# Kernel optimization log

Measured on AMD Instinct MI355X. Metric: run time of the kernel, lower is better.

## Reference

```python
import jax, jax.numpy as jnp
import numpy as np

B, T = 64, 512
IN, OUT, H = 256, 256, 1024


def _lstm_cell(x, h, c, Wih, Whh, bih, bhh):
    # PyTorch LSTMCell: gates = x@Wih^T + bih + h@Whh^T + bhh, order i,f,g,o
    gates = x @ Wih.T + bih + h @ Whh.T + bhh
    i, f, g, o = jnp.split(gates, 4, axis=-1)
    c_new = jax.nn.sigmoid(f) * c + jax.nn.sigmoid(i) * jnp.tanh(g)
    h_new = jax.nn.sigmoid(o) * jnp.tanh(c_new)
    return h_new, c_new


def setup_inputs() -> dict:
    key = jax.random.key(0)
    ks = jax.random.split(key, 12)
    s = 1.0 / np.sqrt(H)  # torch default uniform(-1/sqrt(H), 1/sqrt(H))
    u = lambda k, shp: jax.random.uniform(k, shp, jnp.float32, -s, s)
    return {
        "z": jax.random.normal(ks[0], (B, H), jnp.float32),
        "x": jax.random.normal(ks[1], (B, T, IN), jnp.float32),
        "Wih0": u(ks[2], (4 * H, IN)),
        "Whh0": u(ks[3], (4 * H, H)),
        "bih0": u(ks[4], (4 * H,)),
        "bhh0": u(ks[5], (4 * H,)),
        "Wih1": u(ks[6], (4 * H, H)),
        "Whh1": u(ks[7], (4 * H, H)),
        "bih1": u(ks[8], (4 * H,)),
        "bhh1": u(ks[9], (4 * H,)),
        "Wlin": u(ks[10], (OUT, H)),
        "blin": u(ks[11], (OUT,)),
    }


def reference(z, x, Wih0, Whh0, bih0, bhh0, Wih1, Whh1, bih1, bhh1, Wlin, blin):
    # Teacher-forcing unroll: h_t[l] init to z, c_t[l] init to 0, first input is zeros,
    # then input at step t+1 is x[:, t].
    x_tb = jnp.swapaxes(x, 0, 1)  # [T, B, IN]
    c0_init = jnp.zeros_like(z)

    def step(carry, x_t):
        cur_in, h0, c0, h1, c1 = carry
        h0, c0 = _lstm_cell(cur_in, h0, c0, Wih0, Whh0, bih0, bhh0)
        h1, c1 = _lstm_cell(h0, h1, c1, Wih1, Whh1, bih1, bhh1)
        out_t = h1 @ Wlin.T + blin  # [B, OUT]
        return (x_t, h0, c0, h1, c1), out_t

    init = (jnp.zeros((z.shape[0], Wih0.shape[1]), z.dtype), z, c0_init, z, c0_init)
    _, outs = jax.lax.scan(step, init, x_tb)  # outs: [T, B, OUT]
    return jnp.swapaxes(outs, 0, 1)  # [B, T, OUT]
```

## Files before the change

kernel.cpp:

```cpp
#include <hip/hip_runtime.h>
#include <hip/hip_bf16.h>
#include <math.h>


typedef __attribute__((ext_vector_type(8))) short bf16x8;
typedef __attribute__((ext_vector_type(4))) float f32x4;

__device__ __forceinline__ float sigm(float v) { return 1.f / (1.f + expf(-v)); }

__device__ __forceinline__ void vstore_bf16(__hip_bfloat16* p, float v) {
  __hip_bfloat16 hb = __float2bfloat16(v);
  unsigned short us;
  __builtin_memcpy(&us, &hb, 2);
  *(volatile unsigned short*)p = us;
}


__global__ __launch_bounds__(256) void prep_w0(const float* __restrict__ Wih0,
                                               const float* __restrict__ Whh0,
                                               __hip_bfloat16* __restrict__ W0) {
  const unsigned n = 4096u * 1280u;
  for (unsigned d = blockIdx.x * blockDim.x + threadIdx.x; d < n;
       d += blockDim.x * gridDim.x) {
    unsigned r = d / 1280u;
    unsigned k = d - r * 1280u;
    unsigned u = r >> 2, g = r & 3u;
    unsigned srow = g * 1024u + u;
    float v = (k < 256u) ? Wih0[(size_t)srow * 256u + k]
                         : Whh0[(size_t)srow * 1024u + (k - 256u)];
    W0[d] = __float2bfloat16(v);
  }
}

__global__ __launch_bounds__(256) void prep_w1(const float* __restrict__ Wih1,
                                               const float* __restrict__ Whh1,
                                               const float* __restrict__ Wlin,
                                               __hip_bfloat16* __restrict__ W1) {
  const unsigned n = 4352u * 2048u;
  for (unsigned d = blockIdx.x * blockDim.x + threadIdx.x; d < n;
       d += blockDim.x * gridDim.x) {
    unsigned r = d >> 11;
    unsigned k = d & 2047u;
    float v;
    if (r < 4096u) {
      unsigned u = r >> 2, g = r & 3u;
      unsigned srow = g * 1024u + u;
      v = (k < 1024u) ? Wih1[(size_t)srow * 1024u + k]
                      : Whh1[(size_t)srow * 1024u + (k - 1024u)];
    } else {
      unsigned o = r - 4096u;
      v = (k < 1024u) ? 0.f : Wlin[(size_t)o * 1024u + (k - 1024u)];
    }
    W1[d] = __float2bfloat16(v);
  }
}

__global__ __launch_bounds__(256) void prep_x(const float* __restrict__ x,
                                              __hip_bfloat16* __restrict__ xbf) {
  const unsigned n = 512u * 64u * 256u;
  for (unsigned d = blockIdx.x * blockDim.x + threadIdx.x; d < n;
       d += blockDim.x * gridDim.x) {
    unsigned t = d >> 14;
    unsigned b = (d >> 8) & 63u;
    unsigned k = d & 255u;
    float v = (t == 0u) ? 0.f : x[((size_t)b * 512u + (t - 1u)) * 256u + k];
    xbf[d] = __float2bfloat16(v);
  }
}

__global__ __launch_bounds__(256) void prep_misc(
    const float* __restrict__ bih0, const float* __restrict__ bhh0,
    const float* __restrict__ bih1, const float* __restrict__ bhh1,
    const float* __restrict__ z, float* __restrict__ b0, float* __restrict__ b1,
    __hip_bfloat16* __restrict__ h0buf, __hip_bfloat16* __restrict__ h1buf) {
  for (int i = blockIdx.x * blockDim.x + threadIdx.x; i < 73728;
       i += blockDim.x * gridDim.x) {
    if (i < 4096) {
      int u = i >> 2, g = i & 3;
      b0[i] = bih0[g * 1024 + u] + bhh0[g * 1024 + u];
    } else if (i < 8192) {
      int r = i - 4096;
      int u = r >> 2, g = r & 3;
      b1[r] = bih1[g * 1024 + u] + bhh1[g * 1024 + u];
    } else {
      int j = i - 8192;
      float zv = z[j];
      vstore_bf16(h0buf + j, zv);
      vstore_bf16(h1buf + 2 * 65536 + j, zv);
    }
  }
}


__device__ __forceinline__ void bar_arrive(unsigned* __restrict__ root,
                                           unsigned* __restrict__ lvl,
                                           int phase, int tid) {
  __builtin_amdgcn_s_waitcnt(0);
  __syncthreads();
  if (tid == 0) {
    unsigned old = __hip_atomic_fetch_add(lvl, 1u, __ATOMIC_RELAXED,
                                          __HIP_MEMORY_SCOPE_AGENT);
    if (old == (unsigned)phase * 32u + 31u)
      __hip_atomic_fetch_add(root, 1u, __ATOMIC_RELAXED,
                             __HIP_MEMORY_SCOPE_AGENT);
  }
}

__device__ __forceinline__ void bar_wait(unsigned* __restrict__ root, int phase,
                                         int tid) {
  if (tid == 0) {
    const unsigned tgt = (unsigned)(phase + 1) * 8u;
    while (__hip_atomic_load(root, __ATOMIC_RELAXED,
                             __HIP_MEMORY_SCOPE_AGENT) < tgt)
      __builtin_amdgcn_s_sleep(2);
    __builtin_amdgcn_fence(__ATOMIC_ACQUIRE, "agent");
  }
  __syncthreads();
}


__device__ __forceinline__ void do_proj(const __hip_bfloat16* __restrict__ h1p,
                                        const bf16x8* wp, float (*red)[16][68],
                                        const float* __restrict__ blin,
                                        float* __restrict__ out, int pb,
                                        int t_out, int tid, int w, int col,
                                        int kq) {
  f32x4 a0 = {0.f, 0.f, 0.f, 0.f}, a1 = a0, a2 = a0, a3 = a0;
  const __hip_bfloat16* ab = h1p + (w << 7) + (kq << 3);
#pragma unroll
  for (int c = 0; c < 4; ++c) {
    const __hip_bfloat16* p = ab + (c << 5);
    bf16x8 f0 = *(const bf16x8*)(p + ((size_t)col << 10));
    bf16x8 f1 = *(const bf16x8*)(p + ((size_t)(16 + col) << 10));
    bf16x8 f2 = *(const bf16x8*)(p + ((size_t)(32 + col) << 10));
    bf16x8 f3 = *(const bf16x8*)(p + ((size_t)(48 + col) << 10));
    a0 = __builtin_amdgcn_mfma_f32_16x16x32_bf16(f0, wp[c], a0, 0, 0, 0);
    a1 = __builtin_amdgcn_mfma_f32_16x16x32_bf16(f1, wp[c], a1, 0, 0, 0);
    a2 = __builtin_amdgcn_mfma_f32_16x16x32_bf16(f2, wp[c], a2, 0, 0, 0);
    a3 = __builtin_amdgcn_mfma_f32_16x16x32_bf16(f3, wp[c], a3, 0, 0, 0);
  }
  *(f32x4*)&red[w][col][(kq << 2)] = a0;
  *(f32x4*)&red[w][col][16 + (kq << 2)] = a1;
  *(f32x4*)&red[w][col][32 + (kq << 2)] = a2;
  *(f32x4*)&red[w][col][48 + (kq << 2)] = a3;
  __syncthreads();
#pragma unroll
  for (int i = 0; i < 2; ++i) {
    int idx = tid + (i << 9);
    int o_l = idx & 15, b = idx >> 4;
    float v = blin[(pb << 4) + o_l];
#pragma unroll
    for (int ww = 0; ww < 8; ++ww) v += red[ww][o_l][b];
    out[(((size_t)b << 9) + (size_t)t_out) * 256 + (pb << 4) + o_l] = v;
  }
  __syncthreads();
}


__global__ __launch_bounds__(512) void k_persist(
    const __hip_bfloat16* __restrict__ xbf, const __hip_bfloat16* __restrict__ W0,
    const __hip_bfloat16* __restrict__ W1, const float* __restrict__ b0,
    const float* __restrict__ b1, const float* __restrict__ blin,
    __hip_bfloat16* __restrict__ h0buf, __hip_bfloat16* __restrict__ h1buf,
    float* __restrict__ out, unsigned* __restrict__ bar) {
  const int tid = threadIdx.x;
  const int lane = tid & 63;
  const int w = tid >> 6;
  const int bid = blockIdx.x;
  const int cb = bid << 4;
  const int col = lane & 15;
  const int kq = lane >> 4;
  const int n = cb + col;
  const bool isproj = (bid < 16);

  bf16x8 wa[5], wb[8], wp[4];
  {
    const __hip_bfloat16* p = W0 + (size_t)n * 1280 + w * 160 + (kq << 3);
#pragma unroll
    for (int c = 0; c < 5; ++c) wa[c] = *(const bf16x8*)(p + (c << 5));
  }
  {
    const __hip_bfloat16* p = W1 + ((size_t)n << 11) + (w << 8) + (kq << 3);
#pragma unroll
    for (int c = 0; c < 8; ++c) wb[c] = *(const bf16x8*)(p + (c << 5));
  }
  if (isproj) {
    const __hip_bfloat16* p =
        W1 + ((size_t)(4096 + cb + col) << 11) + 1024 + (w << 7) + (kq << 3);
#pragma unroll
    for (int c = 0; c < 4; ++c) wp[c] = *(const bf16x8*)(p + (c << 5));
  } else {
#pragma unroll
    for (int c = 0; c < 4; ++c) wp[c] = bf16x8{0, 0, 0, 0, 0, 0, 0, 0};
  }

  const int u_l = tid & 3, bq = tid >> 2;
  float bias0[4], bias1[4];
  if (tid < 256) {
#pragma unroll
    for (int g = 0; g < 4; ++g) {
      bias0[g] = b0[cb + (u_l << 2) + g];
      bias1[g] = b1[cb + (u_l << 2) + g];
    }
  }
  float c0v = 0.f, c1v = 0.f;

  __shared__ float red[8][16][68];

  unsigned* lvl = bar + 16 + ((bid & 7) << 6);

  for (int t = 0; t < 512; ++t) {
    const __hip_bfloat16* h0prev = h0buf + ((size_t)(t & 1) << 16);
    const __hip_bfloat16* h0cur = h0buf + ((size_t)((t + 1) & 1) << 16);
    const __hip_bfloat16* h1prev = h1buf + ((size_t)((t + 2) % 3) << 16);
    const __hip_bfloat16* h1proj = h1buf + ((size_t)((t + 1) % 3) << 16);

    {
      f32x4 a0 = {0.f, 0.f, 0.f, 0.f}, a1 = a0, a2 = a0, a3 = a0;
#pragma unroll
      for (int c = 0; c < 5; ++c) {
        const int k0 = w * 160 + (c << 5);
        const __hip_bfloat16* ab;
        size_t rs;
        if (k0 < 256) {
          ab = xbf + ((size_t)t << 14) + k0 + (kq << 3);
          rs = 256;
        } else {
          ab = h0prev + (k0 - 256) + (kq << 3);
          rs = 1024;
        }
        bf16x8 f0 = *(const bf16x8*)(ab + (size_t)col * rs);
        bf16x8 f1 = *(const bf16x8*)(ab + (size_t)(16 + col) * rs);
        bf16x8 f2 = *(const bf16x8*)(ab + (size_t)(32 + col) * rs);
        bf16x8 f3 = *(const bf16x8*)(ab + (size_t)(48 + col) * rs);
        a0 = __builtin_amdgcn_mfma_f32_16x16x32_bf16(f0, wa[c], a0, 0, 0, 0);
        a1 = __builtin_amdgcn_mfma_f32_16x16x32_bf16(f1, wa[c], a1, 0, 0, 0);
        a2 = __builtin_amdgcn_mfma_f32_16x16x32_bf16(f2, wa[c], a2, 0, 0, 0);
        a3 = __builtin_amdgcn_mfma_f32_16x16x32_bf16(f3, wa[c], a3, 0, 0, 0);
      }
      *(f32x4*)&red[w][col][(kq << 2)] = a0;
      *(f32x4*)&red[w][col][16 + (kq << 2)] = a1;
      *(f32x4*)&red[w][col][32 + (kq << 2)] = a2;
      *(f32x4*)&red[w][col][48 + (kq << 2)] = a3;
    }
    __syncthreads();
    if (tid < 256) {
      float gg[4];
#pragma unroll
      for (int g = 0; g < 4; ++g) {
        float v = bias0[g];
#pragma unroll
        for (int ww = 0; ww < 8; ++ww) v += red[ww][(u_l << 2) + g][bq];
        gg[g] = v;
      }
      float cn = sigm(gg[1]) * c0v + sigm(gg[0]) * tanhf(gg[2]);
      c0v = cn;
      float hn = sigm(gg[3]) * tanhf(cn);
      vstore_bf16(h0buf + ((size_t)((t + 1) & 1) << 16) + ((size_t)bq << 10) +
                      (cb >> 2) + u_l,
                  hn);
    }

    bar_arrive(bar, lvl, t, tid);
    if (isproj && t >= 2)
      do_proj(h1proj, wp, red, blin, out, bid, t - 2, tid, w, col, kq);
    bar_wait(bar, t, tid);

    {
      const __hip_bfloat16* ab =
          ((w < 4) ? h0cur : h1prev) + ((w & 3) << 8) + (kq << 3);
      f32x4 a0 = {0.f, 0.f, 0.f, 0.f}, a1 = a0, a2 = a0, a3 = a0;
#pragma unroll
      for (int c = 0; c < 8; ++c) {
        const __hip_bfloat16* p = ab + (c << 5);
        bf16x8 f0 = *(const bf16x8*)(p + ((size_t)col << 10));
        bf16x8 f1 = *(const bf16x8*)(p + ((size_t)(16 + col) << 10));
        bf16x8 f2 = *(const bf16x8*)(p + ((size_t)(32 + col) << 10));
        bf16x8 f3 = *(const bf16x8*)(p + ((size_t)(48 + col) << 10));
        a0 = __builtin_amdgcn_mfma_f32_16x16x32_bf16(f0, wb[c], a0, 0, 0, 0);
        a1 = __builtin_amdgcn_mfma_f32_16x16x32_bf16(f1, wb[c], a1, 0, 0, 0);
        a2 = __builtin_amdgcn_mfma_f32_16x16x32_bf16(f2, wb[c], a2, 0, 0, 0);
        a3 = __builtin_amdgcn_mfma_f32_16x16x32_bf16(f3, wb[c], a3, 0, 0, 0);
      }
      *(f32x4*)&red[w][col][(kq << 2)] = a0;
      *(f32x4*)&red[w][col][16 + (kq << 2)] = a1;
      *(f32x4*)&red[w][col][32 + (kq << 2)] = a2;
      *(f32x4*)&red[w][col][48 + (kq << 2)] = a3;
    }
    __syncthreads();
    if (tid < 256) {
      float gg[4];
#pragma unroll
      for (int g = 0; g < 4; ++g) {
        float v = bias1[g];
#pragma unroll
        for (int ww = 0; ww < 8; ++ww) v += red[ww][(u_l << 2) + g][bq];
        gg[g] = v;
      }
      float cn = sigm(gg[1]) * c1v + sigm(gg[0]) * tanhf(gg[2]);
      c1v = cn;
      float hn = sigm(gg[3]) * tanhf(cn);
      vstore_bf16(h1buf + ((size_t)(t % 3) << 16) + ((size_t)bq << 10) +
                      (cb >> 2) + u_l,
                  hn);
    }
    __syncthreads();
  }

  bar_arrive(bar, lvl, 512, tid);
  bar_wait(bar, 512, tid);
  if (isproj) {
    do_proj(h1buf + ((size_t)(510 % 3) << 16), wp, red, blin, out, bid, 510,
            tid, w, col, kq);
    do_proj(h1buf + ((size_t)(511 % 3) << 16), wp, red, blin, out, bid, 511,
            tid, w, col, kq);
  }
}


extern "C" void kernel_launch(void* const* d_in, const int* in_sizes, int n_in,
                              void* d_out, int out_size, void* d_ws, size_t ws_size,
                              hipStream_t stream) {
  const float* z = (const float*)d_in[0];
  const float* x = (const float*)d_in[1];
  const float* Wih0 = (const float*)d_in[2];
  const float* Whh0 = (const float*)d_in[3];
  const float* bih0 = (const float*)d_in[4];
  const float* bhh0 = (const float*)d_in[5];
  const float* Wih1 = (const float*)d_in[6];
  const float* Whh1 = (const float*)d_in[7];
  const float* bih1 = (const float*)d_in[8];
  const float* bhh1 = (const float*)d_in[9];
  const float* Wlin = (const float*)d_in[10];
  const float* blin = (const float*)d_in[11];
  float* out = (float*)d_out;

  char* ws = (char*)d_ws;
  __hip_bfloat16* W0 = (__hip_bfloat16*)(ws);
  __hip_bfloat16* W1 = (__hip_bfloat16*)(ws + 10485760);
  __hip_bfloat16* xbf = (__hip_bfloat16*)(ws + 28311552);
  float* b0 = (float*)(ws + 45088768);
  float* b1 = (float*)(ws + 45105152);
  __hip_bfloat16* h0buf = (__hip_bfloat16*)(ws + 45121536);
  __hip_bfloat16* h1buf = (__hip_bfloat16*)(ws + 45383680);
  unsigned* bar = (unsigned*)(ws + 45776896);

  hipMemsetAsync(bar, 0, 4096, stream);
  prep_w0<<<4096, 256, 0, stream>>>(Wih0, Whh0, W0);
  prep_w1<<<4096, 256, 0, stream>>>(Wih1, Whh1, Wlin, W1);
  prep_x<<<4096, 256, 0, stream>>>(x, xbf);
  prep_misc<<<288, 256, 0, stream>>>(bih0, bhh0, bih1, bhh1, z, b0, b1, h0buf,
                                     h1buf);

  k_persist<<<256, 512, 0, stream>>>(xbf, W0, W1, b0, b1, blin, h0buf, h1buf,
                                     out, bar);
}
```

Baseline: 10.11 ms.

## Replace hierarchical atomic barrier with per-block flag polling and staged h stores

Replaces the two-level atomic-counter grid barrier with per-block step flags that each block publishes and that one wavefront polls for all 256 blocks with wide atomic loads. Hidden states are staged in shared memory and written as 64-bit atomic stores, and the h1 write for step t is deferred into the next step's h0 publish, so one flag covers both. The output projection is spread over 64 blocks (16 column tiles by 4 batch tiles) instead of 16, which cuts per-block projection work. The aim is lower barrier latency on the serial recurrent path. The cost is more polling traffic and more delicate buffer-indexing and ordering logic.

Result: no change. 10.28 ms (+1.6%).

```diff
diff --git a/kernel.cpp b/kernel.cpp
--- a/kernel.cpp
+++ b/kernel.cpp
@@ -5,14 +5,19 @@
 
 typedef __attribute__((ext_vector_type(8))) short bf16x8;
 typedef __attribute__((ext_vector_type(4))) float f32x4;
+typedef unsigned long long u64;
 
 __device__ __forceinline__ float sigm(float v) { return 1.f / (1.f + expf(-v)); }
 
-__device__ __forceinline__ void vstore_bf16(__hip_bfloat16* p, float v) {
+__device__ __forceinline__ unsigned short bf16_bits(float v) {
   __hip_bfloat16 hb = __float2bfloat16(v);
   unsigned short us;
   __builtin_memcpy(&us, &hb, 2);
-  *(volatile unsigned short*)p = us;
+  return us;
+}
+
+__device__ __forceinline__ void vstore_bf16(__hip_bfloat16* p, float v) {
+  *(volatile unsigned short*)p = bf16_bits(v);
 }
 
 
@@ -92,68 +97,30 @@
 }
 
 
-__device__ __forceinline__ void bar_arrive(unsigned* __restrict__ root,
-                                           unsigned* __restrict__ lvl,
-                                           int phase, int tid) {
-  __builtin_amdgcn_s_waitcnt(0);
-  __syncthreads();
-  if (tid == 0) {
-    unsigned old = __hip_atomic_fetch_add(lvl, 1u, __ATOMIC_RELAXED,
-                                          __HIP_MEMORY_SCOPE_AGENT);
-    if (old == (unsigned)phase * 32u + 31u)
-      __hip_atomic_fetch_add(root, 1u, __ATOMIC_RELAXED,
-                             __HIP_MEMORY_SCOPE_AGENT);
-  }
-}
-
-__device__ __forceinline__ void bar_wait(unsigned* __restrict__ root, int phase,
-                                         int tid) {
-  if (tid == 0) {
-    const unsigned tgt = (unsigned)(phase + 1) * 8u;
-    while (__hip_atomic_load(root, __ATOMIC_RELAXED,
-                             __HIP_MEMORY_SCOPE_AGENT) < tgt)
-      __builtin_amdgcn_s_sleep(2);
-    __builtin_amdgcn_fence(__ATOMIC_ACQUIRE, "agent");
-  }
-  __syncthreads();
-}
-
-
 __device__ __forceinline__ void do_proj(const __hip_bfloat16* __restrict__ h1p,
                                         const bf16x8* wp, float (*red)[16][68],
                                         const float* __restrict__ blin,
-                                        float* __restrict__ out, int pb,
-                                        int t_out, int tid, int w, int col,
-                                        int kq) {
-  f32x4 a0 = {0.f, 0.f, 0.f, 0.f}, a1 = a0, a2 = a0, a3 = a0;
-  const __hip_bfloat16* ab = h1p + (w << 7) + (kq << 3);
+                                        float* __restrict__ out, int pcol,
+                                        int pbat, int t_out, int tid, int w,
+                                        int col, int kq) {
+  f32x4 a0 = {0.f, 0.f, 0.f, 0.f};
+  const __hip_bfloat16* ab =
+      h1p + ((size_t)((pbat << 4) + col) << 10) + (w << 7) + (kq << 3);
 #pragma unroll
   for (int c = 0; c < 4; ++c) {
-    const __hip_bfloat16* p = ab + (c << 5);
-    bf16x8 f0 = *(const bf16x8*)(p + ((size_t)col << 10));
-    bf16x8 f1 = *(const bf16x8*)(p + ((size_t)(16 + col) << 10));
-    bf16x8 f2 = *(const bf16x8*)(p + ((size_t)(32 + col) << 10));
-    bf16x8 f3 = *(const bf16x8*)(p + ((size_t)(48 + col) << 10));
-    a0 = __builtin_amdgcn_mfma_f32_16x16x32_bf16(f0, wp[c], a0, 0, 0, 0);
-    a1 = __builtin_amdgcn_mfma_f32_16x16x32_bf16(f1, wp[c], a1, 0, 0, 0);
-    a2 = __builtin_amdgcn_mfma_f32_16x16x32_bf16(f2, wp[c], a2, 0, 0, 0);
-    a3 = __builtin_amdgcn_mfma_f32_16x16x32_bf16(f3, wp[c], a3, 0, 0, 0);
+    bf16x8 f = *(const bf16x8*)(ab + (c << 5));
+    a0 = __builtin_amdgcn_mfma_f32_16x16x32_bf16(f, wp[c], a0, 0, 0, 0);
   }
   *(f32x4*)&red[w][col][(kq << 2)] = a0;
-  *(f32x4*)&red[w][col][16 + (kq << 2)] = a1;
-  *(f32x4*)&red[w][col][32 + (kq << 2)] = a2;
-  *(f32x4*)&red[w][col][48 + (kq << 2)] = a3;
   __syncthreads();
-#pragma unroll
-  for (int i = 0; i < 2; ++i) {
-    int idx = tid + (i << 9);
-    int o_l = idx & 15, b = idx >> 4;
-    float v = blin[(pb << 4) + o_l];
+  if (tid < 256) {
+    int o_l = tid & 15, b = tid >> 4;
+    float v = blin[(pcol << 4) + o_l];
 #pragma unroll
     for (int ww = 0; ww < 8; ++ww) v += red[ww][o_l][b];
-    out[(((size_t)b << 9) + (size_t)t_out) * 256 + (pb << 4) + o_l] = v;
-  }
-  __syncthreads();
+    out[(((size_t)((pbat << 4) + b) << 9) + (size_t)t_out) * 256 + (pcol << 4) +
+        o_l] = v;
+  }
 }
 
 
@@ -162,7 +129,7 @@
     const __hip_bfloat16* __restrict__ W1, const float* __restrict__ b0,
     const float* __restrict__ b1, const float* __restrict__ blin,
     __hip_bfloat16* __restrict__ h0buf, __hip_bfloat16* __restrict__ h1buf,
-    float* __restrict__ out, unsigned* __restrict__ bar) {
+    float* __restrict__ out, unsigned* __restrict__ flags) {
   const int tid = threadIdx.x;
   const int lane = tid & 63;
   const int w = tid >> 6;
@@ -171,7 +138,9 @@
   const int col = lane & 15;
   const int kq = lane >> 4;
   const int n = cb + col;
-  const bool isproj = (bid < 16);
+  const bool isproj = (bid < 64);
+  const int pcol = bid & 15;
+  const int pbat = (bid >> 4) & 3;
 
   bf16x8 wa[5], wb[8], wp[4];
   {
@@ -185,13 +154,10 @@
     for (int c = 0; c < 8; ++c) wb[c] = *(const bf16x8*)(p + (c << 5));
   }
   if (isproj) {
-    const __hip_bfloat16* p =
-        W1 + ((size_t)(4096 + cb + col) << 11) + 1024 + (w << 7) + (kq << 3);
+    const __hip_bfloat16* p = W1 +
+        ((size_t)(4096 + (pcol << 4) + col) << 11) + 1024 + (w << 7) + (kq << 3);
 #pragma unroll
     for (int c = 0; c < 4; ++c) wp[c] = *(const bf16x8*)(p + (c << 5));
-  } else {
-#pragma unroll
-    for (int c = 0; c < 4; ++c) wp[c] = bf16x8{0, 0, 0, 0, 0, 0, 0, 0};
   }
 
   const int u_l = tid & 3, bq = tid >> 2;
@@ -206,14 +172,13 @@
   float c0v = 0.f, c1v = 0.f;
 
   __shared__ float red[8][16][68];
-
-  unsigned* lvl = bar + 16 + ((bid & 7) << 6);
+  __shared__ unsigned short hst0[64][4];
+  __shared__ unsigned short hst1[64][4];
 
   for (int t = 0; t < 512; ++t) {
     const __hip_bfloat16* h0prev = h0buf + ((size_t)(t & 1) << 16);
     const __hip_bfloat16* h0cur = h0buf + ((size_t)((t + 1) & 1) << 16);
     const __hip_bfloat16* h1prev = h1buf + ((size_t)((t + 2) % 3) << 16);
-    const __hip_bfloat16* h1proj = h1buf + ((size_t)((t + 1) % 3) << 16);
 
     {
       f32x4 a0 = {0.f, 0.f, 0.f, 0.f}, a1 = a0, a2 = a0, a3 = a0;
@@ -255,16 +220,50 @@
       }
       float cn = sigm(gg[1]) * c0v + sigm(gg[0]) * tanhf(gg[2]);
       c0v = cn;
-      float hn = sigm(gg[3]) * tanhf(cn);
-      vstore_bf16(h0buf + ((size_t)((t + 1) & 1) << 16) + ((size_t)bq << 10) +
-                      (cb >> 2) + u_l,
-                  hn);
-    }
-
-    bar_arrive(bar, lvl, t, tid);
+      hst0[bq][u_l] = bf16_bits(sigm(gg[3]) * tanhf(cn));
+    }
+    __syncthreads();
+
+    if (w == 0) {
+      u64 v0;
+      __builtin_memcpy(&v0, &hst0[lane][0], 8);
+      __hip_atomic_store((u64*)(h0buf + (((size_t)((t + 1) & 1)) << 16) +
+                                ((size_t)lane << 10) + (cb >> 2)),
+                         v0, __ATOMIC_RELAXED, __HIP_MEMORY_SCOPE_AGENT);
+      if (t > 0) {
+        u64 v1;
+        __builtin_memcpy(&v1, &hst1[lane][0], 8);
+        __hip_atomic_store((u64*)(h1buf + (((size_t)((t + 2) % 3)) << 16) +
+                                  ((size_t)lane << 10) + (cb >> 2)),
+                           v1, __ATOMIC_RELAXED, __HIP_MEMORY_SCOPE_AGENT);
+      }
+      __builtin_amdgcn_s_waitcnt(0);
+      __builtin_amdgcn_sched_barrier(0);
+      if (lane == 0)
+        __hip_atomic_store(&flags[bid], (unsigned)(t + 1), __ATOMIC_RELAXED,
+                           __HIP_MEMORY_SCOPE_AGENT);
+    }
+
     if (isproj && t >= 2)
-      do_proj(h1proj, wp, red, blin, out, bid, t - 2, tid, w, col, kq);
-    bar_wait(bar, t, tid);
+      do_proj(h1buf + (((size_t)((t + 1) % 3)) << 16), wp, red, blin, out,
+              pcol, pbat, t - 2, tid, w, col, kq);
+
+    if (w == 0) {
+      const unsigned tgt = (unsigned)(t + 1);
+      const u64* fq = (const u64*)flags;
+      for (;;) {
+        u64 q0 = __hip_atomic_load(&fq[2 * lane], __ATOMIC_RELAXED,
+                                   __HIP_MEMORY_SCOPE_AGENT);
+        u64 q1 = __hip_atomic_load(&fq[2 * lane + 1], __ATOMIC_RELAXED,
+                                   __HIP_MEMORY_SCOPE_AGENT);
+        int ok = ((unsigned)q0 >= tgt) & ((unsigned)(q0 >> 32) >= tgt) &
+                 ((unsigned)q1 >= tgt) & ((unsigned)(q1 >> 32) >= tgt);
+        if (__all(ok)) break;
+        __builtin_amdgcn_s_sleep(1);
+      }
+      __builtin_amdgcn_fence(__ATOMIC_ACQUIRE, "agent");
+    }
+    __syncthreads();
 
     {
       const __hip_bfloat16* ab =
@@ -299,22 +298,44 @@
       }
       float cn = sigm(gg[1]) * c1v + sigm(gg[0]) * tanhf(gg[2]);
       c1v = cn;
-      float hn = sigm(gg[3]) * tanhf(cn);
-      vstore_bf16(h1buf + ((size_t)(t % 3) << 16) + ((size_t)bq << 10) +
-                      (cb >> 2) + u_l,
-                  hn);
-    }
-    __syncthreads();
-  }
-
-  bar_arrive(bar, lvl, 512, tid);
-  bar_wait(bar, 512, tid);
-  if (isproj) {
-    do_proj(h1buf + ((size_t)(510 % 3) << 16), wp, red, blin, out, bid, 510,
-            tid, w, col, kq);
-    do_proj(h1buf + ((size_t)(511 % 3) << 16), wp, red, blin, out, bid, 511,
-            tid, w, col, kq);
-  }
+      hst1[bq][u_l] = bf16_bits(sigm(gg[3]) * tanhf(cn));
+    }
+    __syncthreads();
+  }
+
+  if (isproj)
+    do_proj(h1buf, wp, red, blin, out, pcol, pbat, 510, tid, w, col, kq);
+
+  if (w == 0) {
+    u64 v1;
+    __builtin_memcpy(&v1, &hst1[lane][0], 8);
+    __hip_atomic_store((u64*)(h1buf + ((size_t)3 << 16) +
+                              ((size_t)lane << 10) + (cb >> 2)),
+                       v1, __ATOMIC_RELAXED, __HIP_MEMORY_SCOPE_AGENT);
+    __builtin_amdgcn_s_waitcnt(0);
+    __builtin_amdgcn_sched_barrier(0);
+    if (lane == 0)
+      __hip_atomic_store(&flags[bid], 513u, __ATOMIC_RELAXED,
+                         __HIP_MEMORY_SCOPE_AGENT);
+  }
+  if (!isproj) return;
+  if (w == 0) {
+    const u64* fq = (const u64*)flags;
+    for (;;) {
+      u64 q0 = __hip_atomic_load(&fq[2 * lane], __ATOMIC_RELAXED,
+                                 __HIP_MEMORY_SCOPE_AGENT);
+      u64 q1 = __hip_atomic_load(&fq[2 * lane + 1], __ATOMIC_RELAXED,
+                                 __HIP_MEMORY_SCOPE_AGENT);
+      int ok = ((unsigned)q0 >= 513u) & ((unsigned)(q0 >> 32) >= 513u) &
+               ((unsigned)q1 >= 513u) & ((unsigned)(q1 >> 32) >= 513u);
+      if (__all(ok)) break;
+      __builtin_amdgcn_s_sleep(1);
+    }
+    __builtin_amdgcn_fence(__ATOMIC_ACQUIRE, "agent");
+  }
+  __syncthreads();
+  do_proj(h1buf + ((size_t)3 << 16), wp, red, blin, out, pcol, pbat, 511, tid,
+          w, col, kq);
 }
 
 
@@ -343,9 +364,9 @@
   float* b1 = (float*)(ws + 45105152);
   __hip_bfloat16* h0buf = (__hip_bfloat16*)(ws + 45121536);
   __hip_bfloat16* h1buf = (__hip_bfloat16*)(ws + 45383680);
-  unsigned* bar = (unsigned*)(ws + 45776896);
-
-  hipMemsetAsync(bar, 0, 4096, stream);
+  unsigned* flags = (unsigned*)(ws + 45907968);
+
+  hipMemsetAsync(flags, 0, 4096, stream);
   prep_w0<<<4096, 256, 0, stream>>>(Wih0, Whh0, W0);
   prep_w1<<<4096, 256, 0, stream>>>(Wih1, Whh1, Wlin, W1);
   prep_x<<<4096, 256, 0, stream>>>(x, xbf);
@@ -353,5 +374,5 @@
                                      h1buf);
 
   k_persist<<<256, 512, 0, stream>>>(xbf, W0, W1, b0, b1, blin, h0buf, h1buf,
-                                     out, bar);
-}
+                                     out, flags);
+}
```
